# Optimization experiments

Measured on AMD Instinct MI355X. Metric: run time of the kernel, lower is better.

The kernel has to match this reference:

```python
import jax, jax.numpy as jnp
import numpy as np

D_MODEL = 1024
D_INNER = 2048
N_EXPERTS = 8
TOP_K = 2
INIT_STD = 0.02


def setup_inputs() -> dict:
    key = jax.random.key(0)
    ks = jax.random.split(key, 6)
    B, S = 2, 2048
    x = jax.random.normal(ks[0], (B, S, D_MODEL), dtype=jnp.float32)
    router_w = jax.random.normal(ks[1], (N_EXPERTS, D_MODEL), dtype=jnp.float32) * (INIT_STD * 0.1)
    router_b = jnp.zeros((N_EXPERTS,), dtype=jnp.float32)
    gate_w = jax.random.normal(ks[2], (N_EXPERTS, D_MODEL, D_INNER), dtype=jnp.float32) * INIT_STD
    up_w = jax.random.normal(ks[3], (N_EXPERTS, D_MODEL, D_INNER), dtype=jnp.float32) * INIT_STD
    down_w = jax.random.normal(ks[4], (N_EXPERTS, D_INNER, D_MODEL), dtype=jnp.float32) * INIT_STD
    return {"x": x, "router_w": router_w, "router_b": router_b,
            "gate_w": gate_w, "up_w": up_w, "down_w": down_w}


def reference(x, router_w, router_b, gate_w, up_w, down_w):
    # Router: softmax over experts, top-k, renormalize top-k probs.
    logits = jnp.einsum('bsd,ed->bse', x, router_w) + router_b          # [B,S,E]
    probs = jax.nn.softmax(logits, axis=-1)
    top_p, top_i = jax.lax.top_k(probs, TOP_K)                           # [B,S,K]
    top_p = top_p / jnp.sum(top_p, axis=-1, keepdims=True)
    # Per-expert combine weight: c[b,s,e] = sum_k top_p[b,s,k] * [top_i[b,s,k]==e]
    onehot = jax.nn.one_hot(top_i, N_EXPERTS, dtype=x.dtype)             # [B,S,K,E]
    combine = jnp.einsum('bsk,bske->bse', top_p, onehot)                 # [B,S,E]
    # SwiGLU FFN for every expert (dense form of the masked dispatch),
    # zeroed/weighted by combine coefficients.
    g = jnp.einsum('bsd,edf->ebsf', x, gate_w)                           # [E,B,S,F]
    u = jnp.einsum('bsd,edf->ebsf', x, up_w)
    h = jax.nn.silu(g) * u
    y = jnp.einsum('ebsf,efd->ebsd', h, down_w)                          # [E,B,S,D]
    out = jnp.einsum('ebsd,bse->bsd', y, combine)
    return out
```

## Files before the change

kernel.cpp:

```cpp
#include <hip/hip_runtime.h>
#include <hip/hip_bf16.h>
#include <stdint.h>

#define D_MODEL 1024
#define D_INNER 2048
#define NEXP 8
#define TOPK 2
#define BM 128
#define MAXT 72

typedef float f32x4 __attribute__((ext_vector_type(4)));
typedef short bf16x8 __attribute__((ext_vector_type(8)));

#define MEMFENCE asm volatile("" ::: "memory")

__device__ __forceinline__ unsigned short f2b(float f) {
    union { float f; uint32_t u; } v; v.f = f;
    uint32_t u = v.u;
    return (unsigned short)((u + 0x7fffu + ((u >> 16) & 1u)) >> 16);
}

__device__ __forceinline__ void gl_lds16(const void* g, void* l) {
    __builtin_amdgcn_global_load_lds((const __attribute__((address_space(1))) void*)g,
                                     (__attribute__((address_space(3))) void*)l, 16, 0, 0);
}

__global__ __launch_bounds__(256) void cast_x_kernel(
    const float* __restrict__ in, unsigned short* __restrict__ out, int n8)
{
    int i = blockIdx.x * 256 + threadIdx.x;
    if (i >= n8) return;
    const float4* p = (const float4*)(in + (size_t)i * 8);
    float4 a = p[0], b = p[1];
    unsigned short o[8] = {f2b(a.x), f2b(a.y), f2b(a.z), f2b(a.w),
                           f2b(b.x), f2b(b.y), f2b(b.z), f2b(b.w)};
    *(uint4*)(out + (size_t)i * 8) = *(uint4*)o;
}

__global__ __launch_bounds__(256) void tcast_kernel(
    const float* __restrict__ in, unsigned short* __restrict__ out, int K, int N)
{
    __shared__ unsigned short S[64][68];
    int e = blockIdx.z;
    int n0 = blockIdx.x * 64, k0 = blockIdx.y * 64;
    const float* ib = in + (size_t)e * K * N;
    unsigned short* ob = out + (size_t)e * N * K;
    int tid = threadIdx.x;
    int kk = tid >> 4, nn4 = (tid & 15) * 4;
#pragma unroll
    for (int j = 0; j < 4; j++) {
        int k = kk + 16 * j;
        float4 v = *(const float4*)&ib[(size_t)(k0 + k) * N + n0 + nn4];
        ushort4 s; s.x = f2b(v.x); s.y = f2b(v.y); s.z = f2b(v.z); s.w = f2b(v.w);
        *(ushort4*)&S[k][nn4] = s;
    }
    __syncthreads();
    int nn = tid >> 4, kk4 = (tid & 15) * 4;
#pragma unroll
    for (int j = 0; j < 4; j++) {
        int n = nn + 16 * j;
        ushort4 s;
        s.x = S[kk4 + 0][n]; s.y = S[kk4 + 1][n];
        s.z = S[kk4 + 2][n]; s.w = S[kk4 + 3][n];
        *(ushort4*)&ob[(size_t)(n0 + n) * K + k0 + kk4] = s;
    }
}

__global__ __launch_bounds__(64) void router_kernel(
    const float* __restrict__ x, const float* __restrict__ rw,
    const float* __restrict__ rb, int* __restrict__ top_i,
    float* __restrict__ top_w, int T)
{
    int t = blockIdx.x;
    if (t >= T) return;
    int l = threadIdx.x;
    float xv[16];
#pragma unroll
    for (int i = 0; i < 16; i++) xv[i] = x[(size_t)t * D_MODEL + l + 64 * i];
    float logit[NEXP];
#pragma unroll
    for (int e = 0; e < NEXP; e++) {
        float acc = 0.f;
#pragma unroll
        for (int i = 0; i < 16; i++) acc += xv[i] * rw[e * D_MODEL + l + 64 * i];
#pragma unroll
        for (int s = 32; s > 0; s >>= 1) acc += __shfl_xor(acc, s, 64);
        logit[e] = acc + rb[e];
    }
    if (l == 0) {
        int i0 = 0; float m0 = logit[0];
#pragma unroll
        for (int e = 1; e < NEXP; e++) if (logit[e] > m0) { m0 = logit[e]; i0 = e; }
        int i1 = -1; float m1 = -3.0e38f;
#pragma unroll
        for (int e = 0; e < NEXP; e++) {
            if (e == i0) continue;
            if (logit[e] > m1) { m1 = logit[e]; i1 = e; }
        }
        float w0 = 1.f / (1.f + expf(m1 - m0));
        top_i[t * 2 + 0] = i0; top_i[t * 2 + 1] = i1;
        top_w[t * 2 + 0] = w0; top_w[t * 2 + 1] = 1.f - w0;
    }
}

__global__ __launch_bounds__(256) void bucket_kernel(
    const int* __restrict__ top_i, const float* __restrict__ top_w,
    int* __restrict__ meta, int* __restrict__ tok_of_slot,
    float* __restrict__ w_of_slot, int T)
{
    __shared__ int cnt[256][NEXP];
    __shared__ int pre[256][NEXP];
    __shared__ int tot[NEXP];
    __shared__ int off[NEXP + 1];
    int tid = threadIdx.x;
    int per = (T + 255) / 256;
    int t0 = tid * per;
    for (int e = 0; e < NEXP; e++) cnt[tid][e] = 0;
    for (int t = t0; t < t0 + per && t < T; t++)
        for (int k = 0; k < TOPK; k++) cnt[tid][top_i[t * 2 + k]]++;
    __syncthreads();
    if (tid < NEXP) {
        int run = 0;
        for (int i = 0; i < 256; i++) { pre[i][tid] = run; run += cnt[i][tid]; }
        tot[tid] = run;
    }
    __syncthreads();
    if (tid == 0) {
        off[0] = 0;
        for (int e = 0; e < NEXP; e++) off[e + 1] = off[e] + tot[e];
        for (int e = 0; e <= NEXP; e++) meta[e] = off[e];
        int nt = 0;
        for (int e = 0; e < NEXP; e++)
            for (int r = off[e]; r < off[e + 1]; r += BM)
                meta[16 + nt++] = (e << 16) | r;
        for (; nt < MAXT; nt++) meta[16 + nt] = -1;
    }
    __syncthreads();
    int lc[NEXP];
#pragma unroll
    for (int e = 0; e < NEXP; e++) lc[e] = 0;
    for (int t = t0; t < t0 + per && t < T; t++) {
        for (int k = 0; k < TOPK; k++) {
            int e = top_i[t * 2 + k];
            int slot = off[e] + pre[tid][e] + lc[e]++;
            tok_of_slot[slot] = t;
            w_of_slot[slot] = top_w[t * 2 + k];
        }
    }
}

__global__ __launch_bounds__(256, 2) void moe_gate_up(
    const unsigned short* __restrict__ xb, const unsigned short* __restrict__ wgT,
    const unsigned short* __restrict__ wuT, const int* __restrict__ meta,
    const int* __restrict__ tok_of_slot, unsigned short* __restrict__ H)
{
    __shared__ unsigned short As[2][BM * 64];
    __shared__ unsigned short Bg[2][64 * 64];
    __shared__ unsigned short Bu[2][64 * 64];

    int lin = blockIdx.x;
    int xcd = lin & 7, idx = lin >> 3;
    int tix = idx >> 2;
    int f0 = (xcd * 4 + (idx & 3)) * 64;
    int packed = meta[16 + tix];
    if (packed < 0) return;
    int e = packed >> 16, row0 = packed & 0xffff;
    int Mloc = min(BM, meta[e + 1] - row0);

    int tid = threadIdx.x, wv = tid >> 6, lane = tid & 63;
    int l3 = lane >> 3, c3 = lane & 7;

    const unsigned short* srcA[4];
#pragma unroll
    for (int j = 0; j < 4; j++) {
        int r = wv * 32 + j * 8 + l3;
        int slot = row0 + ((r < Mloc) ? r : 0);
        int tok = tok_of_slot[slot];
        srcA[j] = xb + (size_t)tok * D_MODEL + 8 * (c3 ^ (r & 7));
    }
    const unsigned short* srcG[2]; const unsigned short* srcU[2];
#pragma unroll
    for (int j = 0; j < 2; j++) {
        int r = wv * 16 + j * 8 + l3;
        size_t off = (size_t)e * D_MODEL * D_INNER + (size_t)(f0 + r) * D_MODEL + 8 * (c3 ^ (r & 7));
        srcG[j] = wgT + off; srcU[j] = wuT + off;
    }

    int wm = wv >> 1, wn = wv & 1;
    int lrow = lane & 15, kgrp = lane >> 4;
    int swz = lrow & 7;

    f32x4 accg[4][2], accu[4][2];
#pragma unroll
    for (int i = 0; i < 4; i++)
#pragma unroll
        for (int j = 0; j < 2; j++) {
            accg[i][j] = (f32x4){0.f, 0.f, 0.f, 0.f};
            accu[i][j] = (f32x4){0.f, 0.f, 0.f, 0.f};
        }

    int arow[4], brow[2];
#pragma unroll
    for (int fm = 0; fm < 4; fm++) arow[fm] = (wm * 64 + fm * 16 + lrow) * 64;
#pragma unroll
    for (int fn = 0; fn < 2; fn++) brow[fn] = (wn * 32 + fn * 16 + lrow) * 64;

#pragma unroll
    for (int j = 0; j < 4; j++) gl_lds16(srcA[j], As[0] + (wv * 256 + j * 64) * 8);
#pragma unroll
    for (int j = 0; j < 2; j++) {
        gl_lds16(srcG[j], Bg[0] + (wv * 128 + j * 64) * 8);
        gl_lds16(srcU[j], Bu[0] + (wv * 128 + j * 64) * 8);
    }
    MEMFENCE;

    int cur = 0;
    for (int k0 = 0; k0 < D_MODEL; k0 += 64, cur ^= 1) {
        bool more = (k0 + 64 < D_MODEL);
        if (more) {
            int nxt = cur ^ 1, kn = k0 + 64;
#pragma unroll
            for (int j = 0; j < 4; j++) gl_lds16(srcA[j] + kn, As[nxt] + (wv * 256 + j * 64) * 8);
#pragma unroll
            for (int j = 0; j < 2; j++) {
                gl_lds16(srcG[j] + kn, Bg[nxt] + (wv * 128 + j * 64) * 8);
                gl_lds16(srcU[j] + kn, Bu[nxt] + (wv * 128 + j * 64) * 8);
            }
            asm volatile("s_waitcnt vmcnt(8)" ::: "memory");
        } else {
            asm volatile("s_waitcnt vmcnt(0)" ::: "memory");
        }
        __builtin_amdgcn_s_barrier();
        MEMFENCE;

        const unsigned short* Ac = As[cur];
        const unsigned short* Gc = Bg[cur];
        const unsigned short* Uc = Bu[cur];
        __builtin_amdgcn_s_setprio(1);
#pragma unroll
        for (int ks = 0; ks < 2; ks++) {
            int co = 8 * ((4 * ks + kgrp) ^ swz);
            bf16x8 a[4], bg[2], bu[2];
#pragma unroll
            for (int fm = 0; fm < 4; fm++) a[fm] = *(const bf16x8*)&Ac[arow[fm] + co];
#pragma unroll
            for (int fn = 0; fn < 2; fn++) {
                bg[fn] = *(const bf16x8*)&Gc[brow[fn] + co];
                bu[fn] = *(const bf16x8*)&Bu[cur][brow[fn] + co];
            }
#pragma unroll
            for (int fm = 0; fm < 4; fm++)
#pragma unroll
                for (int fn = 0; fn < 2; fn++) {
                    accg[fm][fn] = __builtin_amdgcn_mfma_f32_16x16x32_bf16(a[fm], bg[fn], accg[fm][fn], 0, 0, 0);
                    accu[fm][fn] = __builtin_amdgcn_mfma_f32_16x16x32_bf16(a[fm], bu[fn], accu[fm][fn], 0, 0, 0);
                }
        }
        __builtin_amdgcn_s_setprio(0);
        MEMFENCE;
        asm volatile("s_waitcnt lgkmcnt(0)" ::: "memory");
        __builtin_amdgcn_s_barrier();
        MEMFENCE;
        (void)Uc;
    }

#pragma unroll
    for (int fm = 0; fm < 4; fm++)
#pragma unroll
        for (int fn = 0; fn < 2; fn++)
#pragma unroll
            for (int r = 0; r < 4; r++) {
                int m = wm * 64 + fm * 16 + kgrp * 4 + r;
                if (m < Mloc) {
                    int n = wn * 32 + fn * 16 + lrow;
                    float g = accg[fm][fn][r], u = accu[fm][fn][r];
                    float h = g / (1.f + __expf(-g)) * u;
                    H[(size_t)(row0 + m) * D_INNER + f0 + n] = f2b(h);
                }
            }
}

__global__ __launch_bounds__(256, 2) void moe_down(
    const unsigned short* __restrict__ H, const unsigned short* __restrict__ wdT,
    const int* __restrict__ meta, const int* __restrict__ tok_of_slot,
    const float* __restrict__ w_of_slot, float* __restrict__ out, int S2)
{
    __shared__ unsigned short As[2][BM * 64];
    __shared__ unsigned short Bs[2][BM * 64];
    __shared__ int toks[BM];
    __shared__ float wts[BM];

    int lin = blockIdx.x;
    int d0 = (lin & 7) * BM;
    int tix = lin >> 3;
    int packed = meta[16 + tix];
    if (packed < 0) return;
    int e = packed >> 16, row0 = packed & 0xffff;
    int Mloc = min(BM, meta[e + 1] - row0);

    int tid = threadIdx.x, wv = tid >> 6, lane = tid & 63;
    int l3 = lane >> 3, c3 = lane & 7;
    if (tid < BM) {
        bool v = tid < Mloc;
        toks[tid] = v ? tok_of_slot[row0 + tid] : 0;
        wts[tid] = v ? w_of_slot[row0 + tid] : 0.f;
    }

    const unsigned short* srcA[4]; const unsigned short* srcB[4];
#pragma unroll
    for (int j = 0; j < 4; j++) {
        int r = wv * 32 + j * 8 + l3;
        int slot = min(row0 + r, S2 - 1);
        srcA[j] = H + (size_t)slot * D_INNER + 8 * (c3 ^ (r & 7));
        srcB[j] = wdT + (size_t)e * D_INNER * D_MODEL + (size_t)(d0 + r) * D_INNER + 8 * (c3 ^ (r & 7));
    }

    int wm = wv >> 1, wn = wv & 1;
    int lrow = lane & 15, kgrp = lane >> 4;
    int swz = lrow & 7;

    f32x4 acc[4][4];
#pragma unroll
    for (int i = 0; i < 4; i++)
#pragma unroll
        for (int j = 0; j < 4; j++) acc[i][j] = (f32x4){0.f, 0.f, 0.f, 0.f};

    int arow[4], brow[4];
#pragma unroll
    for (int fm = 0; fm < 4; fm++) arow[fm] = (wm * 64 + fm * 16 + lrow) * 64;
#pragma unroll
    for (int fn = 0; fn < 4; fn++) brow[fn] = (wn * 64 + fn * 16 + lrow) * 64;

#pragma unroll
    for (int j = 0; j < 4; j++) {
        gl_lds16(srcA[j], As[0] + (wv * 256 + j * 64) * 8);
        gl_lds16(srcB[j], Bs[0] + (wv * 256 + j * 64) * 8);
    }
    MEMFENCE;

    int cur = 0;
    for (int k0 = 0; k0 < D_INNER; k0 += 64, cur ^= 1) {
        bool more = (k0 + 64 < D_INNER);
        if (more) {
            int nxt = cur ^ 1, kn = k0 + 64;
#pragma unroll
            for (int j = 0; j < 4; j++) {
                gl_lds16(srcA[j] + kn, As[nxt] + (wv * 256 + j * 64) * 8);
                gl_lds16(srcB[j] + kn, Bs[nxt] + (wv * 256 + j * 64) * 8);
            }
            asm volatile("s_waitcnt vmcnt(8)" ::: "memory");
        } else {
            asm volatile("s_waitcnt vmcnt(0)" ::: "memory");
        }
        __builtin_amdgcn_s_barrier();
        MEMFENCE;

        const unsigned short* Ac = As[cur];
        const unsigned short* Bc = Bs[cur];
        __builtin_amdgcn_s_setprio(1);
#pragma unroll
        for (int ks = 0; ks < 2; ks++) {
            int co = 8 * ((4 * ks + kgrp) ^ swz);
            bf16x8 a[4], b[4];
#pragma unroll
            for (int fm = 0; fm < 4; fm++) a[fm] = *(const bf16x8*)&Ac[arow[fm] + co];
#pragma unroll
            for (int fn = 0; fn < 4; fn++) b[fn] = *(const bf16x8*)&Bc[brow[fn] + co];
#pragma unroll
            for (int fm = 0; fm < 4; fm++)
#pragma unroll
                for (int fn = 0; fn < 4; fn++)
                    acc[fm][fn] = __builtin_amdgcn_mfma_f32_16x16x32_bf16(a[fm], b[fn], acc[fm][fn], 0, 0, 0);
        }
        __builtin_amdgcn_s_setprio(0);
        MEMFENCE;
        asm volatile("s_waitcnt lgkmcnt(0)" ::: "memory");
        __builtin_amdgcn_s_barrier();
        MEMFENCE;
    }

#pragma unroll
    for (int fm = 0; fm < 4; fm++)
#pragma unroll
        for (int fn = 0; fn < 4; fn++)
#pragma unroll
            for (int r = 0; r < 4; r++) {
                int m = wm * 64 + fm * 16 + kgrp * 4 + r;
                if (m < Mloc) {
                    int n = wn * 64 + fn * 16 + lrow;
                    atomicAdd(&out[(size_t)toks[m] * D_MODEL + d0 + n], wts[m] * acc[fm][fn][r]);
                }
            }
}

extern "C" void kernel_launch(void* const* d_in, const int* in_sizes, int n_in,
                              void* d_out, int out_size, void* d_ws, size_t ws_size,
                              hipStream_t stream) {
    const float* x  = (const float*)d_in[0];
    const float* rw = (const float*)d_in[1];
    const float* rb = (const float*)d_in[2];
    const float* gw = (const float*)d_in[3];
    const float* uw = (const float*)d_in[4];
    const float* dw = (const float*)d_in[5];
    float* out = (float*)d_out;

    int T = in_sizes[0] / D_MODEL;
    int S2 = 2 * T;

    char* ws = (char*)d_ws;
    size_t cur = 0;
    auto take = [&](size_t bytes) { char* p = ws + cur; cur = (cur + bytes + 255) & ~(size_t)255; return p; };
    int*   top_i = (int*)take((size_t)S2 * 4);
    float* top_w = (float*)take((size_t)S2 * 4);
    int*   meta  = (int*)take(1024);
    int*   tos   = (int*)take((size_t)S2 * 4);
    float* wos   = (float*)take((size_t)S2 * 4);
    unsigned short* xb  = (unsigned short*)take((size_t)T * D_MODEL * 2);
    unsigned short* wgT = (unsigned short*)take((size_t)NEXP * D_MODEL * D_INNER * 2);
    unsigned short* wuT = (unsigned short*)take((size_t)NEXP * D_MODEL * D_INNER * 2);
    unsigned short* wdT = (unsigned short*)take((size_t)NEXP * D_MODEL * D_INNER * 2);
    unsigned short* H   = (unsigned short*)take((size_t)S2 * D_INNER * 2);

    hipMemsetAsync(d_out, 0, (size_t)out_size * sizeof(float), stream);

    int n8 = T * D_MODEL / 8;
    cast_x_kernel<<<(n8 + 255) / 256, 256, 0, stream>>>(x, xb, n8);
    tcast_kernel<<<dim3(D_INNER / 64, D_MODEL / 64, NEXP), 256, 0, stream>>>(gw, wgT, D_MODEL, D_INNER);
    tcast_kernel<<<dim3(D_INNER / 64, D_MODEL / 64, NEXP), 256, 0, stream>>>(uw, wuT, D_MODEL, D_INNER);
    tcast_kernel<<<dim3(D_MODEL / 64, D_INNER / 64, NEXP), 256, 0, stream>>>(dw, wdT, D_INNER, D_MODEL);

    router_kernel<<<T, 64, 0, stream>>>(x, rw, rb, top_i, top_w, T);
    bucket_kernel<<<1, 256, 0, stream>>>(top_i, top_w, meta, tos, wos, T);

    moe_gate_up<<<MAXT * 32, 256, 0, stream>>>(xb, wgT, wuT, meta, tos, H);
    moe_down<<<MAXT * 8, 256, 0, stream>>>(H, wdT, meta, tos, wos, out, S2);
}
```

Before: 293.8 us.

## Triple-buffer MoE GEMMs with BK=32 and widen gate/up N-tile to 128

Result: faster. 273.1 us (-7.0%).

```diff
diff --git a/kernel.cpp b/kernel.cpp
--- a/kernel.cpp
+++ b/kernel.cpp
@@ -154,125 +154,111 @@
     const unsigned short* __restrict__ wuT, const int* __restrict__ meta,
     const int* __restrict__ tok_of_slot, unsigned short* __restrict__ H)
 {
-    __shared__ unsigned short As[2][BM * 64];
-    __shared__ unsigned short Bg[2][64 * 64];
-    __shared__ unsigned short Bu[2][64 * 64];
+    extern __shared__ __align__(16) unsigned short lds[];
 
     int lin = blockIdx.x;
-    int xcd = lin & 7, idx = lin >> 3;
-    int tix = idx >> 2;
-    int f0 = (xcd * 4 + (idx & 3)) * 64;
+    int strip = (lin & 7) * 2 + ((lin >> 3) & 1);
+    int tix = lin >> 4;
     int packed = meta[16 + tix];
     if (packed < 0) return;
     int e = packed >> 16, row0 = packed & 0xffff;
     int Mloc = min(BM, meta[e + 1] - row0);
+    int f0 = strip * 128;
 
     int tid = threadIdx.x, wv = tid >> 6, lane = tid & 63;
-    int l3 = lane >> 3, c3 = lane & 7;
-
-    const unsigned short* srcA[4];
-#pragma unroll
-    for (int j = 0; j < 4; j++) {
-        int r = wv * 32 + j * 8 + l3;
-        int slot = row0 + ((r < Mloc) ? r : 0);
-        int tok = tok_of_slot[slot];
-        srcA[j] = xb + (size_t)tok * D_MODEL + 8 * (c3 ^ (r & 7));
-    }
-    const unsigned short* srcG[2]; const unsigned short* srcU[2];
+
+    const unsigned short* srcA[2];
+    const unsigned short* srcG[2];
+    const unsigned short* srcU[2];
 #pragma unroll
     for (int j = 0; j < 2; j++) {
-        int r = wv * 16 + j * 8 + l3;
-        size_t off = (size_t)e * D_MODEL * D_INNER + (size_t)(f0 + r) * D_MODEL + 8 * (c3 ^ (r & 7));
-        srcG[j] = wgT + off; srcU[j] = wuT + off;
+        int row = j * 64 + (tid >> 2);
+        int p = tid & 3;
+        int koffA = 8 * (p ^ ((row >> 1) & 3));
+        int slot = row0 + ((row < Mloc) ? row : 0);
+        srcA[j] = xb + (size_t)tok_of_slot[slot] * D_MODEL + koffA;
+        size_t wb = (size_t)e * D_MODEL * D_INNER + (size_t)(f0 + row) * D_MODEL + koffA;
+        srcG[j] = wgT + wb;
+        srcU[j] = wuT + wb;
     }
 
     int wm = wv >> 1, wn = wv & 1;
     int lrow = lane & 15, kgrp = lane >> 4;
-    int swz = lrow & 7;
-
-    f32x4 accg[4][2], accu[4][2];
+    int co = 8 * (kgrp ^ ((lrow >> 1) & 3));
+
+    int arow[4], brow[4];
+#pragma unroll
+    for (int fm = 0; fm < 4; fm++) arow[fm] = (wm * 64 + fm * 16 + lrow) * 32;
+#pragma unroll
+    for (int fn = 0; fn < 4; fn++) brow[fn] = (wn * 64 + fn * 16 + lrow) * 32;
+
+    f32x4 accg[4][4], accu[4][4];
 #pragma unroll
     for (int i = 0; i < 4; i++)
 #pragma unroll
-        for (int j = 0; j < 2; j++) {
+        for (int j = 0; j < 4; j++) {
             accg[i][j] = (f32x4){0.f, 0.f, 0.f, 0.f};
             accu[i][j] = (f32x4){0.f, 0.f, 0.f, 0.f};
         }
 
-    int arow[4], brow[2];
-#pragma unroll
-    for (int fm = 0; fm < 4; fm++) arow[fm] = (wm * 64 + fm * 16 + lrow) * 64;
-#pragma unroll
-    for (int fn = 0; fn < 2; fn++) brow[fn] = (wn * 32 + fn * 16 + lrow) * 64;
-
-#pragma unroll
-    for (int j = 0; j < 4; j++) gl_lds16(srcA[j], As[0] + (wv * 256 + j * 64) * 8);
-#pragma unroll
-    for (int j = 0; j < 2; j++) {
-        gl_lds16(srcG[j], Bg[0] + (wv * 128 + j * 64) * 8);
-        gl_lds16(srcU[j], Bu[0] + (wv * 128 + j * 64) * 8);
-    }
+    auto stage = [&](int u) {
+        int kk = u * 32;
+        unsigned short* base = lds + (u % 3) * 12288;
+#pragma unroll
+        for (int j = 0; j < 2; j++) {
+            int d = (j * 256 + wv * 64) * 8;
+            gl_lds16(srcA[j] + kk, base + d);
+            gl_lds16(srcG[j] + kk, base + 4096 + d);
+            gl_lds16(srcU[j] + kk, base + 8192 + d);
+        }
+    };
+
+    const int NT = D_MODEL / 32;
+    stage(0); stage(1);
     MEMFENCE;
 
-    int cur = 0;
-    for (int k0 = 0; k0 < D_MODEL; k0 += 64, cur ^= 1) {
-        bool more = (k0 + 64 < D_MODEL);
-        if (more) {
-            int nxt = cur ^ 1, kn = k0 + 64;
-#pragma unroll
-            for (int j = 0; j < 4; j++) gl_lds16(srcA[j] + kn, As[nxt] + (wv * 256 + j * 64) * 8);
-#pragma unroll
-            for (int j = 0; j < 2; j++) {
-                gl_lds16(srcG[j] + kn, Bg[nxt] + (wv * 128 + j * 64) * 8);
-                gl_lds16(srcU[j] + kn, Bu[nxt] + (wv * 128 + j * 64) * 8);
+    for (int t = 0; t < NT; ++t) {
+        if (t + 2 < NT) stage(t + 2);
+        int ahead = NT - 1 - t;
+        if (ahead >= 2)      asm volatile("s_waitcnt vmcnt(12)" ::: "memory");
+        else if (ahead == 1) asm volatile("s_waitcnt vmcnt(6)"  ::: "memory");
+        else                 asm volatile("s_waitcnt vmcnt(0)"  ::: "memory");
+        __builtin_amdgcn_s_barrier();
+        MEMFENCE;
+
+        const unsigned short* base = lds + (t % 3) * 12288;
+        bf16x8 a[4], bg[4], bu[4];
+#pragma unroll
+        for (int fm = 0; fm < 4; fm++) a[fm] = *(const bf16x8*)(base + arow[fm] + co);
+#pragma unroll
+        for (int fn = 0; fn < 4; fn++) {
+            bg[fn] = *(const bf16x8*)(base + 4096 + brow[fn] + co);
+            bu[fn] = *(const bf16x8*)(base + 8192 + brow[fn] + co);
+        }
+        __builtin_amdgcn_s_setprio(1);
+#pragma unroll
+        for (int fm = 0; fm < 4; fm++)
+#pragma unroll
+            for (int fn = 0; fn < 4; fn++) {
+                accg[fm][fn] = __builtin_amdgcn_mfma_f32_16x16x32_bf16(a[fm], bg[fn], accg[fm][fn], 0, 0, 0);
+                accu[fm][fn] = __builtin_amdgcn_mfma_f32_16x16x32_bf16(a[fm], bu[fn], accu[fm][fn], 0, 0, 0);
             }
-            asm volatile("s_waitcnt vmcnt(8)" ::: "memory");
-        } else {
-            asm volatile("s_waitcnt vmcnt(0)" ::: "memory");
-        }
-        __builtin_amdgcn_s_barrier();
-        MEMFENCE;
-
-        const unsigned short* Ac = As[cur];
-        const unsigned short* Gc = Bg[cur];
-        const unsigned short* Uc = Bu[cur];
-        __builtin_amdgcn_s_setprio(1);
-#pragma unroll
-        for (int ks = 0; ks < 2; ks++) {
-            int co = 8 * ((4 * ks + kgrp) ^ swz);
-            bf16x8 a[4], bg[2], bu[2];
-#pragma unroll
-            for (int fm = 0; fm < 4; fm++) a[fm] = *(const bf16x8*)&Ac[arow[fm] + co];
-#pragma unroll
-            for (int fn = 0; fn < 2; fn++) {
-                bg[fn] = *(const bf16x8*)&Gc[brow[fn] + co];
-                bu[fn] = *(const bf16x8*)&Bu[cur][brow[fn] + co];
-            }
-#pragma unroll
-            for (int fm = 0; fm < 4; fm++)
-#pragma unroll
-                for (int fn = 0; fn < 2; fn++) {
-                    accg[fm][fn] = __builtin_amdgcn_mfma_f32_16x16x32_bf16(a[fm], bg[fn], accg[fm][fn], 0, 0, 0);
-                    accu[fm][fn] = __builtin_amdgcn_mfma_f32_16x16x32_bf16(a[fm], bu[fn], accu[fm][fn], 0, 0, 0);
-                }
-        }
         __builtin_amdgcn_s_setprio(0);
         MEMFENCE;
         asm volatile("s_waitcnt lgkmcnt(0)" ::: "memory");
         __builtin_amdgcn_s_barrier();
         MEMFENCE;
-        (void)Uc;
     }
 
 #pragma unroll
     for (int fm = 0; fm < 4; fm++)
 #pragma unroll
-        for (int fn = 0; fn < 2; fn++)
+        for (int fn = 0; fn < 4; fn++)
 #pragma unroll
             for (int r = 0; r < 4; r++) {
                 int m = wm * 64 + fm * 16 + kgrp * 4 + r;
                 if (m < Mloc) {
-                    int n = wn * 32 + fn * 16 + lrow;
+                    int n = wn * 64 + fn * 16 + lrow;
                     float g = accg[fm][fn][r], u = accu[fm][fn][r];
                     float h = g / (1.f + __expf(-g)) * u;
                     H[(size_t)(row0 + m) * D_INNER + f0 + n] = f2b(h);
@@ -285,13 +271,12 @@
     const int* __restrict__ meta, const int* __restrict__ tok_of_slot,
     const float* __restrict__ w_of_slot, float* __restrict__ out, int S2)
 {
-    __shared__ unsigned short As[2][BM * 64];
-    __shared__ unsigned short Bs[2][BM * 64];
+    __shared__ unsigned short lds[3 * 8192];
     __shared__ int toks[BM];
     __shared__ float wts[BM];
 
     int lin = blockIdx.x;
-    int d0 = (lin & 7) * BM;
+    int d0 = (lin & 7) * 128;
     int tix = lin >> 3;
     int packed = meta[16 + tix];
     if (packed < 0) return;
@@ -299,25 +284,33 @@
     int Mloc = min(BM, meta[e + 1] - row0);
 
     int tid = threadIdx.x, wv = tid >> 6, lane = tid & 63;
-    int l3 = lane >> 3, c3 = lane & 7;
     if (tid < BM) {
         bool v = tid < Mloc;
         toks[tid] = v ? tok_of_slot[row0 + tid] : 0;
         wts[tid] = v ? w_of_slot[row0 + tid] : 0.f;
     }
 
-    const unsigned short* srcA[4]; const unsigned short* srcB[4];
-#pragma unroll
-    for (int j = 0; j < 4; j++) {
-        int r = wv * 32 + j * 8 + l3;
-        int slot = min(row0 + r, S2 - 1);
-        srcA[j] = H + (size_t)slot * D_INNER + 8 * (c3 ^ (r & 7));
-        srcB[j] = wdT + (size_t)e * D_INNER * D_MODEL + (size_t)(d0 + r) * D_INNER + 8 * (c3 ^ (r & 7));
+    const unsigned short* srcA[2];
+    const unsigned short* srcB[2];
+#pragma unroll
+    for (int j = 0; j < 2; j++) {
+        int row = j * 64 + (tid >> 2);
+        int p = tid & 3;
+        int koff = 8 * (p ^ ((row >> 1) & 3));
+        int slot = min(row0 + row, S2 - 1);
+        srcA[j] = H + (size_t)slot * D_INNER + koff;
+        srcB[j] = wdT + (size_t)e * D_INNER * D_MODEL + (size_t)(d0 + row) * D_INNER + koff;
     }
 
     int wm = wv >> 1, wn = wv & 1;
     int lrow = lane & 15, kgrp = lane >> 4;
-    int swz = lrow & 7;
+    int co = 8 * (kgrp ^ ((lrow >> 1) & 3));
+
+    int arow[4], brow[4];
+#pragma unroll
+    for (int fm = 0; fm < 4; fm++) arow[fm] = (wm * 64 + fm * 16 + lrow) * 32;
+#pragma unroll
+    for (int fn = 0; fn < 4; fn++) brow[fn] = (wn * 64 + fn * 16 + lrow) * 32;
 
     f32x4 acc[4][4];
 #pragma unroll
@@ -325,53 +318,42 @@
 #pragma unroll
         for (int j = 0; j < 4; j++) acc[i][j] = (f32x4){0.f, 0.f, 0.f, 0.f};
 
-    int arow[4], brow[4];
-#pragma unroll
-    for (int fm = 0; fm < 4; fm++) arow[fm] = (wm * 64 + fm * 16 + lrow) * 64;
-#pragma unroll
-    for (int fn = 0; fn < 4; fn++) brow[fn] = (wn * 64 + fn * 16 + lrow) * 64;
-
-#pragma unroll
-    for (int j = 0; j < 4; j++) {
-        gl_lds16(srcA[j], As[0] + (wv * 256 + j * 64) * 8);
-        gl_lds16(srcB[j], Bs[0] + (wv * 256 + j * 64) * 8);
-    }
+    auto stage = [&](int u) {
+        int kk = u * 32;
+        unsigned short* base = lds + (u % 3) * 8192;
+#pragma unroll
+        for (int j = 0; j < 2; j++) {
+            int d = (j * 256 + wv * 64) * 8;
+            gl_lds16(srcA[j] + kk, base + d);
+            gl_lds16(srcB[j] + kk, base + 4096 + d);
+        }
+    };
+
+    const int NT = D_INNER / 32;
+    stage(0); stage(1);
     MEMFENCE;
 
-    int cur = 0;
-    for (int k0 = 0; k0 < D_INNER; k0 += 64, cur ^= 1) {
-        bool more = (k0 + 64 < D_INNER);
-        if (more) {
-            int nxt = cur ^ 1, kn = k0 + 64;
-#pragma unroll
-            for (int j = 0; j < 4; j++) {
-                gl_lds16(srcA[j] + kn, As[nxt] + (wv * 256 + j * 64) * 8);
-                gl_lds16(srcB[j] + kn, Bs[nxt] + (wv * 256 + j * 64) * 8);
-            }
-            asm volatile("s_waitcnt vmcnt(8)" ::: "memory");
-        } else {
-            asm volatile("s_waitcnt vmcnt(0)" ::: "memory");
-        }
+    for (int t = 0; t < NT; ++t) {
+        if (t + 2 < NT) stage(t + 2);
+        int ahead = NT - 1 - t;
+        if (ahead >= 2)      asm volatile("s_waitcnt vmcnt(8)" ::: "memory");
+        else if (ahead == 1) asm volatile("s_waitcnt vmcnt(4)" ::: "memory");
+        else                 asm volatile("s_waitcnt vmcnt(0)" ::: "memory");
         __builtin_amdgcn_s_barrier();
         MEMFENCE;
 
-        const unsigned short* Ac = As[cur];
-        const unsigned short* Bc = Bs[cur];
+        const unsigned short* base = lds + (t % 3) * 8192;
+        bf16x8 a[4], b[4];
+#pragma unroll
+        for (int fm = 0; fm < 4; fm++) a[fm] = *(const bf16x8*)(base + arow[fm] + co);
+#pragma unroll
+        for (int fn = 0; fn < 4; fn++) b[fn] = *(const bf16x8*)(base + 4096 + brow[fn] + co);
         __builtin_amdgcn_s_setprio(1);
 #pragma unroll
-        for (int ks = 0; ks < 2; ks++) {
-            int co = 8 * ((4 * ks + kgrp) ^ swz);
-            bf16x8 a[4], b[4];
-#pragma unroll
-            for (int fm = 0; fm < 4; fm++) a[fm] = *(const bf16x8*)&Ac[arow[fm] + co];
-#pragma unroll
-            for (int fn = 0; fn < 4; fn++) b[fn] = *(const bf16x8*)&Bc[brow[fn] + co];
-#pragma unroll
-            for (int fm = 0; fm < 4; fm++)
-#pragma unroll
-                for (int fn = 0; fn < 4; fn++)
-                    acc[fm][fn] = __builtin_amdgcn_mfma_f32_16x16x32_bf16(a[fm], b[fn], acc[fm][fn], 0, 0, 0);
-        }
+        for (int fm = 0; fm < 4; fm++)
+#pragma unroll
+            for (int fn = 0; fn < 4; fn++)
+                acc[fm][fn] = __builtin_amdgcn_mfma_f32_16x16x32_bf16(a[fm], b[fn], acc[fm][fn], 0, 0, 0);
         __builtin_amdgcn_s_setprio(0);
         MEMFENCE;
         asm volatile("s_waitcnt lgkmcnt(0)" ::: "memory");
@@ -421,6 +403,10 @@
     unsigned short* wdT = (unsigned short*)take((size_t)NEXP * D_MODEL * D_INNER * 2);
     unsigned short* H   = (unsigned short*)take((size_t)S2 * D_INNER * 2);
 
+    static const int GU_LDS = 3 * 12288 * 2;
+    hipFuncSetAttribute((const void*)moe_gate_up,
+                        hipFuncAttributeMaxDynamicSharedMemorySize, GU_LDS);
+
     hipMemsetAsync(d_out, 0, (size_t)out_size * sizeof(float), stream);
 
     int n8 = T * D_MODEL / 8;
@@ -432,6 +418,6 @@
     router_kernel<<<T, 64, 0, stream>>>(x, rw, rb, top_i, top_w, T);
     bucket_kernel<<<1, 256, 0, stream>>>(top_i, top_w, meta, tos, wos, T);
 
-    moe_gate_up<<<MAXT * 32, 256, 0, stream>>>(xb, wgT, wuT, meta, tos, H);
+    moe_gate_up<<<MAXT * 16, 256, GU_LDS, stream>>>(xb, wgT, wuT, meta, tos, H);
     moe_down<<<MAXT * 8, 256, 0, stream>>>(H, wdT, meta, tos, wos, out, S2);
 }
```
